# Kernel optimization log

Measured on AMD Instinct MI355X. Metric: run time of the kernel, lower is better.

The kernel has to match this reference:

```python
import jax, jax.numpy as jnp
import numpy as np

# Static video grid (F, H, W); S = F*H*W tokens.
F_FRAMES, H_GRID, W_GRID = 9, 16, 28
DIM, N_HEADS = 1536, 12
HEAD_DIM = DIM // N_HEADS          # 128
ROT = HEAD_DIM // 2                # 64 complex pairs
EPS = 1e-6


def setup_inputs() -> dict:
    key = jax.random.key(0)
    ks = jax.random.split(key, 12)
    S = F_FRAMES * H_GRID * W_GRID
    scale = 0.02
    inp = {
        "x": jax.random.normal(ks[0], (1, S, DIM), jnp.float32),
        "seq_lens": jnp.array([S], jnp.int32),
        "grid_sizes": jnp.array([[F_FRAMES, H_GRID, W_GRID]], jnp.int32),
        "freqs": jax.random.normal(ks[1], (1024, ROT), jnp.float32),  # rope angles
        "Wq": jax.random.normal(ks[2], (DIM, DIM), jnp.float32) * scale,
        "bq": jnp.zeros((DIM,), jnp.float32),
        "Wk": jax.random.normal(ks[3], (DIM, DIM), jnp.float32) * scale,
        "bk": jnp.zeros((DIM,), jnp.float32),
        "Wv": jax.random.normal(ks[4], (DIM, DIM), jnp.float32) * scale,
        "bv": jnp.zeros((DIM,), jnp.float32),
        "Wo": jax.random.normal(ks[5], (DIM, DIM), jnp.float32) * scale,
        "bo": jnp.zeros((DIM,), jnp.float32),
        "gq": jnp.ones((DIM,), jnp.float32),
        "gk": jnp.ones((DIM,), jnp.float32),
    }
    return inp


def _rms_norm(h, g):
    # WanRMSNorm: h * rsqrt(mean(h^2) + eps) * weight
    var = jnp.mean(jnp.square(h), axis=-1, keepdims=True)
    return h * jax.lax.rsqrt(var + EPS) * g


def _rope_angles(freqs):
    # Split channel dim into temporal / height / width parts.
    c = ROT
    t_dim = c - 2 * (c // 3)  # 22
    s1 = c // 3               # 21
    temporal, height, width = freqs[:, :t_dim], freqs[:, t_dim:t_dim + s1], freqs[:, t_dim + s1:]
    t_ang = jnp.repeat(temporal[:F_FRAMES], H_GRID * W_GRID, axis=0)         # [S, 22]
    h_ang = jnp.tile(jnp.repeat(height[:H_GRID], W_GRID, axis=0), (F_FRAMES, 1))  # [S, 21]
    w_ang = jnp.tile(jnp.tile(width[:W_GRID], (H_GRID, 1)), (F_FRAMES, 1))        # [S, 21]
    return jnp.concatenate([t_ang, h_ang, w_ang], axis=-1)  # [S, c]


def _rope_apply(x, ang):
    # x: [B, S, n, d] viewed as complex pairs [B, S, n, d/2, 2]
    b, s, n, d = x.shape
    xp = x.reshape(b, s, n, d // 2, 2)
    xr, xi = xp[..., 0], xp[..., 1]
    cos = jnp.cos(ang)[None, :, None, :]
    sin = jnp.sin(ang)[None, :, None, :]
    out_r = xr * cos - xi * sin
    out_i = xr * sin + xi * cos
    return jnp.stack([out_r, out_i], axis=-1).reshape(b, s, n, d)


def reference(x, seq_lens, grid_sizes, freqs, Wq, bq, Wk, bk, Wv, bv, Wo, bo, gq, gk):
    b, s, _ = x.shape
    n, d = N_HEADS, HEAD_DIM
    q = _rms_norm(x @ Wq + bq, gq).reshape(b, s, n, d)
    k = _rms_norm(x @ Wk + bk, gk).reshape(b, s, n, d)
    v = (x @ Wv + bv).reshape(b, s, n, d)

    ang = _rope_angles(freqs)  # [S, d/2]
    rq = _rope_apply(q, ang)
    rk = _rope_apply(k, ang)

    # Causal frame-block mask: query in frame i attends to kv in frames <= i.
    frame_idx = jnp.arange(s) // (H_GRID * W_GRID)
    mask = frame_idx[None, :] <= frame_idx[:, None]  # [S_q, S_k]

    scale = 1.0 / jnp.sqrt(jnp.asarray(d, x.dtype))
    scores = jnp.einsum("bqnd,bknd->bnqk", rq, rk) * scale
    scores = jnp.where(mask[None, None], scores, jnp.asarray(-1e30, scores.dtype))
    probs = jax.nn.softmax(scores, axis=-1)
    attn = jnp.einsum("bnqk,bknd->bqnd", probs, v).reshape(b, s, n * d)
    return attn @ Wo + bo
```

## Files before the change

kernel.cpp:

```cpp
#include <hip/hip_runtime.h>
#include <stdint.h>

typedef unsigned short u16;
typedef unsigned int u32;
typedef __attribute__((ext_vector_type(8))) short bf16x8;
typedef __attribute__((ext_vector_type(4))) float f32x4;

#define S_LEN 4032
#define S_PAD 4096
#define DIMC  1536
#define HD    128
#define FRAME 448

static const size_t OFF_FLAG  = 0;
static const size_t OFF_CANON = 256;
static const size_t OFF_XB    = 524288;
static const size_t OFF_WT    = OFF_XB  + 12582912;
static const size_t OFF_WOT   = OFF_WT  + 14155776;
static const size_t OFF_YQ    = OFF_WOT + 4718592;
static const size_t OFF_YK    = OFF_YQ  + 12582912;
static const size_t OFF_VT    = OFF_YK  + 12582912;
static const size_t OFF_QH    = OFF_VT  + 12582912;
static const size_t OFF_KH    = OFF_QH  + 12386304;
static const size_t OFF_AT    = OFF_KH  + 12386304;
static const size_t WS_NEED   = OFF_AT  + 12582912;

#define C_BQ 0
#define C_BO 4608
#define C_GQ 6144
#define C_GK 7680
#define C_FR 9216
#define C_TOT 74752

__device__ __forceinline__ u16 f2bf(float f) {
  union { float f; u32 u; } v; v.f = f;
  u32 u = v.u;
  u32 r = (u + 0x7fffu + ((u >> 16) & 1u)) >> 16;
  return (u16)r;
}
__device__ __forceinline__ float bf2f(u16 h) {
  union { float f; u32 u; } v; v.u = ((u32)h) << 16;
  return v.f;
}

__device__ __forceinline__ void gld_lds16(const void* g, void* l) {
  __builtin_amdgcn_global_load_lds(
      (const __attribute__((address_space(1))) void*)(uintptr_t)g,
      (__attribute__((address_space(3))) void*)(u32)(uintptr_t)l,
      16, 0, 0);
}

__device__ __forceinline__ f32x4 mfma16(bf16x8 a, bf16x8 b, f32x4 c) {
  return __builtin_amdgcn_mfma_f32_16x16x32_bf16(a, b, c, 0, 0, 0);
}

__global__ void prep_all(const void* __restrict__ x,
                         const void* Wq, const void* Wk, const void* Wv, const void* Wo,
                         const void* bq, const void* bk, const void* bv, const void* bo,
                         const void* gq, const void* gk, const void* fr,
                         float* __restrict__ canon, u16* __restrict__ xb,
                         u16* __restrict__ wqkvt, u16* __restrict__ wot,
                         int* __restrict__ flag) {
  __shared__ int cnt;
  __shared__ float tile[32][33];
  const int tid = threadIdx.x;
  if (tid == 0) cnt = 0;
  __syncthreads();
  int e = (((const u16*)x)[2 * tid] >> 7) & 0xff;
  if (e > 150) atomicAdd(&cnt, 1);
  __syncthreads();
  const int fl = (cnt >= 8) ? 1 : 0;
  const int bid = blockIdx.x;
  if (bid == 0 && tid == 0) *flag = fl;

  if (bid < 9216) {
    const int z = bid / 2304;
    const int rem = bid % 2304;
    const int by = rem / 48, bx = rem % 48;
    const void* W = (z == 0) ? Wq : (z == 1) ? Wk : (z == 2) ? Wv : Wo;
    u16* dst = (z < 3) ? (wqkvt + (size_t)z * DIMC * DIMC) : wot;
    const int tx = tid & 31, ty = tid >> 5;
    const int c = bx * 32 + tx;
    #pragma unroll
    for (int i = 0; i < 4; i++) {
      int r = by * 32 + ty + i * 8;
      float v = fl ? ((const float*)W)[(size_t)r * DIMC + c]
                   : bf2f(((const u16*)W)[(size_t)r * DIMC + c]);
      tile[ty + i * 8][tx] = v;
    }
    __syncthreads();
    const int k = by * 32 + tx;
    #pragma unroll
    for (int i = 0; i < 4; i++) {
      int n = bx * 32 + ty + i * 8;
      dst[(size_t)n * DIMC + k] = f2bf(tile[tx][ty + i * 8]);
    }
  } else if (bid < 12288) {
    int i = (bid - 9216) * 256 + tid;
    if (i < (S_PAD * DIMC) / 8) {
      size_t base = (size_t)i * 8;
      int row = (int)(base / DIMC);
      union { u16 h[8]; uint4 v; } u;
      if (row < S_LEN) {
        if (fl) {
          const float* xf = (const float*)x + base;
          #pragma unroll
          for (int j = 0; j < 8; j++) u.h[j] = f2bf(xf[j]);
        } else {
          const u16* xh = (const u16*)x + base;
          #pragma unroll
          for (int j = 0; j < 8; j++) u.h[j] = xh[j];
        }
      } else {
        #pragma unroll
        for (int j = 0; j < 8; j++) u.h[j] = 0;
      }
      ((uint4*)xb)[i] = u.v;
    }
  } else {
    for (int i = (bid - 12288) * 256 + tid; i < C_TOT; i += 292 * 256) {
      const void* src; int j;
      if      (i < 1536) { src = bq; j = i; }
      else if (i < 3072) { src = bk; j = i - 1536; }
      else if (i < 4608) { src = bv; j = i - 3072; }
      else if (i < 6144) { src = bo; j = i - 4608; }
      else if (i < 7680) { src = gq; j = i - 6144; }
      else if (i < 9216) { src = gk; j = i - 7680; }
      else               { src = fr; j = i - 9216; }
      canon[i] = fl ? ((const float*)src)[j] : bf2f(((const u16*)src)[j]);
    }
  }
}

template <int MODE>
__launch_bounds__(256, 4)
__global__ void gemm_bt(const u16* __restrict__ A, const u16* __restrict__ Bt,
                        const float* __restrict__ canon,
                        u16* __restrict__ Yq, u16* __restrict__ Yk, u16* __restrict__ Vt,
                        void* __restrict__ Out, const int* __restrict__ flagp) {
  const int bm0 = blockIdx.y * 128, bn0 = blockIdx.x * 128;
  const int tid = threadIdx.x, wave = tid >> 6, lane = tid & 63;
  const int wm = wave >> 1, wn = wave & 1;
  const int l15 = lane & 15, l4 = lane >> 4;
  __shared__ u16 sA[128 * 64];
  __shared__ u16 sB[128 * 64];
  f32x4 acc[4][4];
  #pragma unroll
  for (int i = 0; i < 4; i++)
    #pragma unroll
    for (int j = 0; j < 4; j++) acc[i][j] = (f32x4){0.f, 0.f, 0.f, 0.f};

  const int swc = ((lane & 7) ^ (lane >> 3)) * 8;
  const u16* Ab = A  + (size_t)(bm0 + (lane >> 3)) * DIMC + swc;
  const u16* Bb = Bt + (size_t)(bn0 + (lane >> 3)) * DIMC + swc;

  for (int kt = 0; kt < DIMC; kt += 64) {
    __syncthreads();
    #pragma unroll
    for (int c = 0; c < 4; c++) {
      int g = wave * 4 + c;
      gld_lds16(Ab + (size_t)g * 8 * DIMC + kt, (char*)sA + g * 1024);
      gld_lds16(Bb + (size_t)g * 8 * DIMC + kt, (char*)sB + g * 1024);
    }
    __syncthreads();
    #pragma unroll
    for (int ks = 0; ks < 2; ks++) {
      bf16x8 av[4], bvv[4];
      #pragma unroll
      for (int mt = 0; mt < 4; mt++)
        av[mt]  = *(const bf16x8*)(sA + (wm * 64 + mt * 16 + l15) * 64 +
                                   (((ks * 4 + l4) ^ (l15 & 7)) * 8));
      #pragma unroll
      for (int nt = 0; nt < 4; nt++)
        bvv[nt] = *(const bf16x8*)(sB + (wn * 64 + nt * 16 + l15) * 64 +
                                   (((ks * 4 + l4) ^ (l15 & 7)) * 8));
      #pragma unroll
      for (int mt = 0; mt < 4; mt++)
        #pragma unroll
        for (int nt = 0; nt < 4; nt++)
          acc[mt][nt] = mfma16(av[mt], bvv[nt], acc[mt][nt]);
    }
  }

  const int gm0 = bm0 + wm * 64;
  const int gn0 = bn0 + wn * 64;
  if (MODE == 0) {
    #pragma unroll
    for (int nt = 0; nt < 4; nt++) {
      int gn = gn0 + nt * 16 + l15;
      float b = canon[C_BQ + gn];
      #pragma unroll
      for (int mt = 0; mt < 4; mt++) {
        int gm = gm0 + mt * 16 + l4 * 4;
        if (gn < 1536) {
          #pragma unroll
          for (int r = 0; r < 4; r++)
            Yq[(size_t)(gm + r) * DIMC + gn] = f2bf(acc[mt][nt][r] + b);
        } else if (gn < 3072) {
          int g2 = gn - 1536;
          #pragma unroll
          for (int r = 0; r < 4; r++)
            Yk[(size_t)(gm + r) * DIMC + g2] = f2bf(acc[mt][nt][r] + b);
        } else {
          int g2 = gn - 3072;
          u32 lo = (u32)f2bf(acc[mt][nt][0] + b) | ((u32)f2bf(acc[mt][nt][1] + b) << 16);
          u32 hi = (u32)f2bf(acc[mt][nt][2] + b) | ((u32)f2bf(acc[mt][nt][3] + b) << 16);
          uint2 pk; pk.x = lo; pk.y = hi;
          *(uint2*)(Vt + (size_t)g2 * S_PAD + gm) = pk;
        }
      }
    }
  } else {
    const int fl = *flagp;
    #pragma unroll
    for (int nt = 0; nt < 4; nt++) {
      int gn = gn0 + nt * 16 + l15;
      float b = canon[C_BO + gn];
      #pragma unroll
      for (int mt = 0; mt < 4; mt++) {
        int gm = gm0 + mt * 16 + l4 * 4;
        #pragma unroll
        for (int r = 0; r < 4; r++) {
          int gr = gm + r;
          if (gr < S_LEN) {
            float v = acc[mt][nt][r] + b;
            if (fl) ((float*)Out)[(size_t)gr * DIMC + gn] = v;
            else    ((u16*)Out)[(size_t)gr * DIMC + gn] = f2bf(v);
          }
        }
      }
    }
  }
}

__global__ void norm_rope(const u16* __restrict__ Yq, const u16* __restrict__ Yk,
                          const float* __restrict__ canon, u16* __restrict__ Qh,
                          u16* __restrict__ Kh) {
  const int tid = threadIdx.x, wave = tid >> 6, lane = tid & 63;
  const int s = blockIdx.x * 4 + wave;
  const int isq = (blockIdx.y == 0);
  const u16* Y = isq ? Yq : Yk;
  const float* g = canon + (isq ? C_GQ : C_GK);
  u16* Oh = isq ? Qh : Kh;
  const float sc = isq ? (0.08838834764831845f * 1.4426950408889634f) : 1.0f;

  const u32* yrow = (const u32*)Y + (size_t)s * 768;
  float xr[12], xi[12];
  float ss = 0.f;
  #pragma unroll
  for (int i = 0; i < 12; i++) {
    u32 d = yrow[lane + 64 * i];
    float a = bf2f((u16)(d & 0xffff));
    float b = bf2f((u16)(d >> 16));
    xr[i] = a; xi[i] = b;
    ss += a * a + b * b;
  }
  #pragma unroll
  for (int dd = 1; dd < 64; dd <<= 1) ss += __shfl_xor(ss, dd, 64);
  float rms = rsqrtf(ss * (1.f / 1536.f) + 1e-6f);

  int f_ = s / FRAME, hh = (s % FRAME) / 28, ww = s % 28;
  const float* fr = canon + C_FR;
  float a = (lane < 22) ? fr[f_ * 64 + lane]
          : (lane < 43) ? fr[hh * 64 + lane]
                        : fr[ww * 64 + lane];
  float si, co;
  __sincosf(a, &si, &co);

  const float2* g2 = (const float2*)g;
  #pragma unroll
  for (int i = 0; i < 12; i++) {
    int p = lane + 64 * i;
    float2 gg = g2[p];
    float r  = xr[i] * rms * gg.x;
    float im = xi[i] * rms * gg.y;
    u32 pk = (u32)f2bf((r * co - im * si) * sc) | ((u32)f2bf((r * si + im * co) * sc) << 16);
    ((u32*)Oh)[((size_t)i * S_LEN + s) * 64 + lane] = pk;
  }
}

__launch_bounds__(256, 2)
__global__ void attn_v5(const u16* __restrict__ Qh, const u16* __restrict__ Kh,
                        const u16* __restrict__ Vt, u16* __restrict__ Ab) {
  const int tid = threadIdx.x, wave = tid >> 6, lane = tid & 63;
  const int l15 = lane & 15, l4 = lane >> 4;
  const int pair = wave >> 1, m = wave & 1;
  const int h = blockIdx.x % 12;
  const int qb = 62 - (blockIdx.x / 12);
  const int q0 = qb * 64;
  const int nkv = (q0 / FRAME + 1) * 7;
  __shared__ u16 sK[2][8192];
  __shared__ u16 sV[2][8192];
  __shared__ u16 sP[8][1024];

  int koff[8], voff[8];
  #pragma unroll
  for (int i = 0; i < 8; i++) {
    int c = i * 128 + m * 64 + lane;
    int r = c >> 4, cc = (c & 15) ^ (r & 15);
    koff[i] = r * HD + cc * 8;
    int rv = c >> 3, cv = (c & 7) ^ (rv & 7);
    voff[i] = rv * S_PAD + cv * 8;
  }

  bf16x8 qf[4][2];
  #pragma unroll
  for (int ct = 0; ct < 2; ct++) {
    const u16* qp = Qh + ((size_t)h * S_LEN + q0 + m * 32 + ct * 16 + l15) * HD + l4 * 8;
    #pragma unroll
    for (int ks = 0; ks < 4; ks++) qf[ks][ct] = *(const bf16x8*)(qp + ks * 32);
  }
  f32x4 o[8][2];
  #pragma unroll
  for (int i = 0; i < 8; i++)
    #pragma unroll
    for (int ct = 0; ct < 2; ct++) o[i][ct] = (f32x4){0.f, 0.f, 0.f, 0.f};
  float l_i[2] = {0.f, 0.f};

  const u16* kb0 = Kh + (size_t)h * S_LEN * HD;
  const u16* vb0 = Vt + (size_t)h * HD * S_PAD;
  const int niter = (nkv + 1) >> 1;

  for (int it = 0; it < niter; ++it) {
    const int t = it * 2 + pair;
    const bool active = (t < nkv);
    __syncthreads();
    if (active) {
      const u16* kb = kb0 + (size_t)t * 64 * HD;
      const u16* vb = vb0 + t * 64;
      #pragma unroll
      for (int i = 0; i < 8; i++) {
        gld_lds16(kb + koff[i], (char*)sK[pair] + i * 2048 + m * 1024);
        gld_lds16(vb + voff[i], (char*)sV[pair] + i * 2048 + m * 1024);
      }
    }
    __syncthreads();
    if (!active) continue;

    f32x4 sT[4][2];
    #pragma unroll
    for (int nt = 0; nt < 4; nt++)
      #pragma unroll
      for (int ct = 0; ct < 2; ct++) sT[nt][ct] = (f32x4){0.f, 0.f, 0.f, 0.f};
    #pragma unroll
    for (int ks = 0; ks < 4; ks++) {
      bf16x8 kf[4];
      #pragma unroll
      for (int nt = 0; nt < 4; nt++)
        kf[nt] = *(const bf16x8*)(sK[pair] + (nt * 16 + l15) * HD + (((ks * 4 + l4) ^ l15) * 8));
      #pragma unroll
      for (int nt = 0; nt < 4; nt++)
        #pragma unroll
        for (int ct = 0; ct < 2; ct++)
          sT[nt][ct] = mfma16(kf[nt], qf[ks][ct], sT[nt][ct]);
    }

    #pragma unroll
    for (int ct = 0; ct < 2; ct++) {
      float rs = 0.f;
      #pragma unroll
      for (int nt = 0; nt < 4; nt++)
        #pragma unroll
        for (int r = 0; r < 4; r++) {
          float p = __builtin_amdgcn_exp2f(sT[nt][ct][r]);
          sT[nt][ct][r] = p; rs += p;
        }
      l_i[ct] += rs;
      u16* pw = sP[wave * 2 + ct];
      #pragma unroll
      for (int nt = 0; nt < 4; nt++) {
        u32 lo = (u32)f2bf(sT[nt][ct][0]) | ((u32)f2bf(sT[nt][ct][1]) << 16);
        u32 hi = (u32)f2bf(sT[nt][ct][2]) | ((u32)f2bf(sT[nt][ct][3]) << 16);
        u32 off = (u32)((nt >> 1) * 512 + ((nt & 1) * 2 + (l4 >> 1)) * 128 + l15 * 8 + (l4 & 1) * 4);
        uint2 pk; pk.x = lo; pk.y = hi;
        *(uint2*)(pw + off) = pk;
      }
    }

    #pragma unroll
    for (int ks2 = 0; ks2 < 2; ks2++) {
      bf16x8 pb[2];
      #pragma unroll
      for (int ct = 0; ct < 2; ct++)
        pb[ct] = *(const bf16x8*)(sP[wave * 2 + ct] + ks2 * 512 + lane * 8);
      #pragma unroll
      for (int vt = 0; vt < 8; vt++) {
        bf16x8 vf = *(const bf16x8*)(sV[pair] + (vt * 16 + l15) * 64 + (((ks2 * 4 + l4) ^ (l15 & 7)) * 8));
        #pragma unroll
        for (int ct = 0; ct < 2; ct++)
          o[vt][ct] = mfma16(vf, pb[ct], o[vt][ct]);
      }
    }
  }

  #pragma unroll
  for (int ct = 0; ct < 2; ct++) {
    l_i[ct] += __shfl_xor(l_i[ct], 16, 64);
    l_i[ct] += __shfl_xor(l_i[ct], 32, 64);
  }
  __syncthreads();
  float* mb = (float*)sK;
  float* lb = (float*)sP;
  if (pair == 1) {
    #pragma unroll
    for (int ct = 0; ct < 2; ct++) {
      #pragma unroll
      for (int vt = 0; vt < 8; vt++)
        *(f32x4*)(mb + m * 4096 + (ct * 8 + vt) * 256 + lane * 4) = o[vt][ct];
      lb[m * 128 + ct * 64 + lane] = l_i[ct];
    }
  }
  __syncthreads();
  if (pair == 0) {
    #pragma unroll
    for (int ct = 0; ct < 2; ct++) {
      float l = l_i[ct] + lb[m * 128 + ct * 64 + lane];
      float inv = 1.f / l;
      const size_t orow = (size_t)(q0 + m * 32 + ct * 16 + l15) * DIMC + (size_t)h * HD;
      #pragma unroll
      for (int vt = 0; vt < 8; vt++) {
        f32x4 op = *(const f32x4*)(mb + m * 4096 + (ct * 8 + vt) * 256 + lane * 4);
        float o0 = (o[vt][ct][0] + op[0]) * inv;
        float o1 = (o[vt][ct][1] + op[1]) * inv;
        float o2 = (o[vt][ct][2] + op[2]) * inv;
        float o3 = (o[vt][ct][3] + op[3]) * inv;
        u32 lo = (u32)f2bf(o0) | ((u32)f2bf(o1) << 16);
        u32 hi = (u32)f2bf(o2) | ((u32)f2bf(o3) << 16);
        uint2 pk; pk.x = lo; pk.y = hi;
        *(uint2*)(Ab + orow + vt * 16 + l4 * 4) = pk;
      }
    }
  }
}

extern "C" void kernel_launch(void* const* d_in, const int* in_sizes, int n_in,
                              void* d_out, int out_size, void* d_ws, size_t ws_size,
                              hipStream_t stream) {
  if (ws_size < WS_NEED) return;
  char* ws = (char*)d_ws;
  int*   flag  = (int*)(ws + OFF_FLAG);
  float* canon = (float*)(ws + OFF_CANON);
  u16* xb    = (u16*)(ws + OFF_XB);
  u16* wqkvt = (u16*)(ws + OFF_WT);
  u16* wot   = (u16*)(ws + OFF_WOT);
  u16* yq    = (u16*)(ws + OFF_YQ);
  u16* yk    = (u16*)(ws + OFF_YK);
  u16* vt    = (u16*)(ws + OFF_VT);
  u16* qh    = (u16*)(ws + OFF_QH);
  u16* kh    = (u16*)(ws + OFF_KH);
  u16* ab    = (u16*)(ws + OFF_AT);

  const void* x  = d_in[0];
  const void* fr = d_in[3];
  const void* Wq = d_in[4];  const void* bq = d_in[5];
  const void* Wk = d_in[6];  const void* bk = d_in[7];
  const void* Wv = d_in[8];  const void* bv = d_in[9];
  const void* Wo = d_in[10]; const void* bo = d_in[11];
  const void* gq = d_in[12]; const void* gk = d_in[13];

  prep_all<<<12580, 256, 0, stream>>>(x, Wq, Wk, Wv, Wo, bq, bk, bv, bo, gq, gk, fr,
                                      canon, xb, wqkvt, wot, flag);
  gemm_bt<0><<<dim3(36, 32), 256, 0, stream>>>(xb, wqkvt, canon, yq, yk, vt, nullptr, flag);
  norm_rope<<<dim3(1008, 2), 256, 0, stream>>>(yq, yk, canon, qh, kh);
  attn_v5<<<756, 256, 0, stream>>>(qh, kh, vt, ab);
  gemm_bt<1><<<dim3(12, 32), 256, 0, stream>>>(ab, wot, canon, nullptr, nullptr, nullptr, d_out, flag);
}
```

Before: 343.6 us.

## Restructure attention into 7-wave blocks of 112 queries sharing each KV tile

The attention kernel moves from 4-wave blocks of 64 queries, where two wave pairs split the KV tiles and merged their partial outputs through LDS, to 7-wave blocks of 112 queries. Each wave owns 16 query rows and every wave consumes the same KV tile, so the cross-pair reduction goes away and each loaded K/V tile is reused by more query rows. Since 112 rows divide the 448-token frame exactly, no block spans a frame boundary. The grid drops from 756 to 432 blocks, and s_setprio hints are placed around the MFMA sections. The trade-off is fewer blocks and a single LDS K/V buffer with no double buffering, so load latency may be less well hidden.

```diff
diff --git a/kernel.cpp b/kernel.cpp
--- a/kernel.cpp
+++ b/kernel.cpp
@@ -279,157 +279,113 @@
   }
 }
 
-__launch_bounds__(256, 2)
-__global__ void attn_v5(const u16* __restrict__ Qh, const u16* __restrict__ Kh,
+__launch_bounds__(448, 4)
+__global__ void attn_v6(const u16* __restrict__ Qh, const u16* __restrict__ Kh,
                         const u16* __restrict__ Vt, u16* __restrict__ Ab) {
   const int tid = threadIdx.x, wave = tid >> 6, lane = tid & 63;
   const int l15 = lane & 15, l4 = lane >> 4;
-  const int pair = wave >> 1, m = wave & 1;
   const int h = blockIdx.x % 12;
-  const int qb = 62 - (blockIdx.x / 12);
-  const int q0 = qb * 64;
+  const int qb = 35 - (blockIdx.x / 12);
+  const int q0 = qb * 112;
   const int nkv = (q0 / FRAME + 1) * 7;
-  __shared__ u16 sK[2][8192];
-  __shared__ u16 sV[2][8192];
-  __shared__ u16 sP[8][1024];
-
-  int koff[8], voff[8];
-  #pragma unroll
-  for (int i = 0; i < 8; i++) {
-    int c = i * 128 + m * 64 + lane;
+  __shared__ u16 sK[8192];
+  __shared__ u16 sV[8192];
+  __shared__ u16 sP[7][1024];
+
+  int koff[3], voff[3];
+  #pragma unroll
+  for (int i = 0; i < 3; i++) {
+    int c = i * 448 + tid;
     int r = c >> 4, cc = (c & 15) ^ (r & 15);
     koff[i] = r * HD + cc * 8;
     int rv = c >> 3, cv = (c & 7) ^ (rv & 7);
     voff[i] = rv * S_PAD + cv * 8;
   }
 
-  bf16x8 qf[4][2];
-  #pragma unroll
-  for (int ct = 0; ct < 2; ct++) {
-    const u16* qp = Qh + ((size_t)h * S_LEN + q0 + m * 32 + ct * 16 + l15) * HD + l4 * 8;
-    #pragma unroll
-    for (int ks = 0; ks < 4; ks++) qf[ks][ct] = *(const bf16x8*)(qp + ks * 32);
-  }
-  f32x4 o[8][2];
-  #pragma unroll
-  for (int i = 0; i < 8; i++)
-    #pragma unroll
-    for (int ct = 0; ct < 2; ct++) o[i][ct] = (f32x4){0.f, 0.f, 0.f, 0.f};
-  float l_i[2] = {0.f, 0.f};
+  bf16x8 qf[4];
+  {
+    const u16* qp = Qh + ((size_t)h * S_LEN + q0 + wave * 16 + l15) * HD + l4 * 8;
+    #pragma unroll
+    for (int ks = 0; ks < 4; ks++) qf[ks] = *(const bf16x8*)(qp + ks * 32);
+  }
+  f32x4 o[8];
+  #pragma unroll
+  for (int i = 0; i < 8; i++) o[i] = (f32x4){0.f, 0.f, 0.f, 0.f};
+  float l_i = 0.f;
 
   const u16* kb0 = Kh + (size_t)h * S_LEN * HD;
   const u16* vb0 = Vt + (size_t)h * HD * S_PAD;
-  const int niter = (nkv + 1) >> 1;
-
-  for (int it = 0; it < niter; ++it) {
-    const int t = it * 2 + pair;
-    const bool active = (t < nkv);
+
+  for (int t = 0; t < nkv; ++t) {
     __syncthreads();
-    if (active) {
-      const u16* kb = kb0 + (size_t)t * 64 * HD;
-      const u16* vb = vb0 + t * 64;
-      #pragma unroll
-      for (int i = 0; i < 8; i++) {
-        gld_lds16(kb + koff[i], (char*)sK[pair] + i * 2048 + m * 1024);
-        gld_lds16(vb + voff[i], (char*)sV[pair] + i * 2048 + m * 1024);
+    const u16* kb = kb0 + (size_t)t * 64 * HD;
+    const u16* vb = vb0 + t * 64;
+    #pragma unroll
+    for (int i = 0; i < 3; i++) {
+      int c = i * 448 + tid;
+      if (c < 1024) {
+        gld_lds16(kb + koff[i], (char*)sK + (size_t)(c - lane) * 16);
+        gld_lds16(vb + voff[i], (char*)sV + (size_t)(c - lane) * 16);
       }
     }
     __syncthreads();
-    if (!active) continue;
-
-    f32x4 sT[4][2];
-    #pragma unroll
-    for (int nt = 0; nt < 4; nt++)
-      #pragma unroll
-      for (int ct = 0; ct < 2; ct++) sT[nt][ct] = (f32x4){0.f, 0.f, 0.f, 0.f};
+
+    f32x4 sT[4];
+    #pragma unroll
+    for (int nt = 0; nt < 4; nt++) sT[nt] = (f32x4){0.f, 0.f, 0.f, 0.f};
+    __builtin_amdgcn_s_setprio(1);
     #pragma unroll
     for (int ks = 0; ks < 4; ks++) {
       bf16x8 kf[4];
       #pragma unroll
       for (int nt = 0; nt < 4; nt++)
-        kf[nt] = *(const bf16x8*)(sK[pair] + (nt * 16 + l15) * HD + (((ks * 4 + l4) ^ l15) * 8));
+        kf[nt] = *(const bf16x8*)(sK + (nt * 16 + l15) * HD + (((ks * 4 + l4) ^ l15) * 8));
       #pragma unroll
       for (int nt = 0; nt < 4; nt++)
-        #pragma unroll
-        for (int ct = 0; ct < 2; ct++)
-          sT[nt][ct] = mfma16(kf[nt], qf[ks][ct], sT[nt][ct]);
-    }
-
-    #pragma unroll
-    for (int ct = 0; ct < 2; ct++) {
-      float rs = 0.f;
-      #pragma unroll
-      for (int nt = 0; nt < 4; nt++)
-        #pragma unroll
-        for (int r = 0; r < 4; r++) {
-          float p = __builtin_amdgcn_exp2f(sT[nt][ct][r]);
-          sT[nt][ct][r] = p; rs += p;
-        }
-      l_i[ct] += rs;
-      u16* pw = sP[wave * 2 + ct];
-      #pragma unroll
-      for (int nt = 0; nt < 4; nt++) {
-        u32 lo = (u32)f2bf(sT[nt][ct][0]) | ((u32)f2bf(sT[nt][ct][1]) << 16);
-        u32 hi = (u32)f2bf(sT[nt][ct][2]) | ((u32)f2bf(sT[nt][ct][3]) << 16);
-        u32 off = (u32)((nt >> 1) * 512 + ((nt & 1) * 2 + (l4 >> 1)) * 128 + l15 * 8 + (l4 & 1) * 4);
-        uint2 pk; pk.x = lo; pk.y = hi;
-        *(uint2*)(pw + off) = pk;
-      }
-    }
+        sT[nt] = mfma16(kf[nt], qf[ks], sT[nt]);
+    }
+    __builtin_amdgcn_s_setprio(0);
+
+    float rs = 0.f;
+    u16* pw = sP[wave];
+    #pragma unroll
+    for (int nt = 0; nt < 4; nt++) {
+      #pragma unroll
+      for (int r = 0; r < 4; r++) {
+        float p = __builtin_amdgcn_exp2f(sT[nt][r]);
+        sT[nt][r] = p; rs += p;
+      }
+      u32 lo = (u32)f2bf(sT[nt][0]) | ((u32)f2bf(sT[nt][1]) << 16);
+      u32 hi = (u32)f2bf(sT[nt][2]) | ((u32)f2bf(sT[nt][3]) << 16);
+      u32 off = (u32)((nt >> 1) * 512 + ((nt & 1) * 2 + (l4 >> 1)) * 128 + l15 * 8 + (l4 & 1) * 4);
+      uint2 pk; pk.x = lo; pk.y = hi;
+      *(uint2*)(pw + off) = pk;
+    }
+    l_i += rs;
 
     #pragma unroll
     for (int ks2 = 0; ks2 < 2; ks2++) {
-      bf16x8 pb[2];
-      #pragma unroll
-      for (int ct = 0; ct < 2; ct++)
-        pb[ct] = *(const bf16x8*)(sP[wave * 2 + ct] + ks2 * 512 + lane * 8);
+      bf16x8 pb = *(const bf16x8*)(sP[wave] + ks2 * 512 + lane * 8);
+      __builtin_amdgcn_s_setprio(1);
       #pragma unroll
       for (int vt = 0; vt < 8; vt++) {
-        bf16x8 vf = *(const bf16x8*)(sV[pair] + (vt * 16 + l15) * 64 + (((ks2 * 4 + l4) ^ (l15 & 7)) * 8));
-        #pragma unroll
-        for (int ct = 0; ct < 2; ct++)
-          o[vt][ct] = mfma16(vf, pb[ct], o[vt][ct]);
-      }
-    }
-  }
-
-  #pragma unroll
-  for (int ct = 0; ct < 2; ct++) {
-    l_i[ct] += __shfl_xor(l_i[ct], 16, 64);
-    l_i[ct] += __shfl_xor(l_i[ct], 32, 64);
-  }
-  __syncthreads();
-  float* mb = (float*)sK;
-  float* lb = (float*)sP;
-  if (pair == 1) {
-    #pragma unroll
-    for (int ct = 0; ct < 2; ct++) {
-      #pragma unroll
-      for (int vt = 0; vt < 8; vt++)
-        *(f32x4*)(mb + m * 4096 + (ct * 8 + vt) * 256 + lane * 4) = o[vt][ct];
-      lb[m * 128 + ct * 64 + lane] = l_i[ct];
-    }
-  }
-  __syncthreads();
-  if (pair == 0) {
-    #pragma unroll
-    for (int ct = 0; ct < 2; ct++) {
-      float l = l_i[ct] + lb[m * 128 + ct * 64 + lane];
-      float inv = 1.f / l;
-      const size_t orow = (size_t)(q0 + m * 32 + ct * 16 + l15) * DIMC + (size_t)h * HD;
-      #pragma unroll
-      for (int vt = 0; vt < 8; vt++) {
-        f32x4 op = *(const f32x4*)(mb + m * 4096 + (ct * 8 + vt) * 256 + lane * 4);
-        float o0 = (o[vt][ct][0] + op[0]) * inv;
-        float o1 = (o[vt][ct][1] + op[1]) * inv;
-        float o2 = (o[vt][ct][2] + op[2]) * inv;
-        float o3 = (o[vt][ct][3] + op[3]) * inv;
-        u32 lo = (u32)f2bf(o0) | ((u32)f2bf(o1) << 16);
-        u32 hi = (u32)f2bf(o2) | ((u32)f2bf(o3) << 16);
-        uint2 pk; pk.x = lo; pk.y = hi;
-        *(uint2*)(Ab + orow + vt * 16 + l4 * 4) = pk;
-      }
-    }
+        bf16x8 vf = *(const bf16x8*)(sV + (vt * 16 + l15) * 64 + (((ks2 * 4 + l4) ^ (l15 & 7)) * 8));
+        o[vt] = mfma16(vf, pb, o[vt]);
+      }
+      __builtin_amdgcn_s_setprio(0);
+    }
+  }
+
+  l_i += __shfl_xor(l_i, 16, 64);
+  l_i += __shfl_xor(l_i, 32, 64);
+  float inv = 1.f / l_i;
+  const size_t orow = (size_t)(q0 + wave * 16 + l15) * DIMC + (size_t)h * HD;
+  #pragma unroll
+  for (int vt = 0; vt < 8; vt++) {
+    u32 lo = (u32)f2bf(o[vt][0] * inv) | ((u32)f2bf(o[vt][1] * inv) << 16);
+    u32 hi = (u32)f2bf(o[vt][2] * inv) | ((u32)f2bf(o[vt][3] * inv) << 16);
+    uint2 pk; pk.x = lo; pk.y = hi;
+    *(uint2*)(Ab + orow + vt * 16 + l4 * 4) = pk;
   }
 }
 
@@ -462,6 +418,6 @@
                                       canon, xb, wqkvt, wot, flag);
   gemm_bt<0><<<dim3(36, 32), 256, 0, stream>>>(xb, wqkvt, canon, yq, yk, vt, nullptr, flag);
   norm_rope<<<dim3(1008, 2), 256, 0, stream>>>(yq, yk, canon, qh, kh);
-  attn_v5<<<756, 256, 0, stream>>>(qh, kh, vt, ab);
+  attn_v6<<<432, 448, 0, stream>>>(qh, kh, vt, ab);
   gemm_bt<1><<<dim3(12, 32), 256, 0, stream>>>(ab, wot, canon, nullptr, nullptr, nullptr, d_out, flag);
 }
```

Result: slower. 371.6 us (+8.2%).
